# Kernel optimization log

Hardware: AMD Instinct MI355X
Metric: run time of the kernel (lower is better)

The kernel has to match this reference:

```python
import jax, jax.numpy as jnp
import numpy as np

QMAX = 127.0

def fake_quant(t):
    # per-tensor symmetric int8 quantize -> dequantize (STE for grads)
    scale = jnp.maximum(jnp.max(jnp.abs(t)) / QMAX, 1e-8)
    q = jnp.clip(jnp.round(t / scale), -QMAX, QMAX) * scale
    return t + jax.lax.stop_gradient(q - t)

def qlinear(x, W, b):
    # quantized linear: int8 activations x int8 weights, dequantized output
    return fake_quant(x) @ fake_quant(W).T + b

def hardsigmoid(t):
    return jnp.clip(t / 6.0 + 0.5, 0.0, 1.0)

def setup_inputs() -> dict:
    key = jax.random.key(0)
    ks = jax.random.split(key, 5)
    B, C, H, W_, R = 64, 1024, 28, 28, 256
    return {
        "x":  jax.random.normal(ks[0], (B, C, H, W_), dtype=jnp.float32),
        "W1": jax.random.normal(ks[1], (R, C), dtype=jnp.float32) * (1.0 / np.sqrt(C)),
        "b1": jax.random.normal(ks[2], (R,), dtype=jnp.float32) * 0.01,
        "W2": jax.random.normal(ks[3], (C, R), dtype=jnp.float32) * (1.0 / np.sqrt(R)),
        "b2": jax.random.normal(ks[4], (C,), dtype=jnp.float32) * 0.01,
    }

def reference(x, W1, b1, W2, b2):
    b, c, h, w = x.shape
    # 1. quantize input
    xq = fake_quant(x)
    # 2. quantized global avgpool -> [b, c]
    se = fake_quant(jnp.mean(xq, axis=(2, 3)))
    # 3-4. quantized fc1 -> fp32 relu
    se = jax.nn.relu(qlinear(se, W1, b1))
    # 5. quantized fc2 -> fp32
    se = qlinear(se, W2, b2)
    # 6. hardsigmoid gate
    se = hardsigmoid(se)
    # 7. broadcast scale in fp32 (original input path was fp32)
    return x * se[:, :, None, None]
```

## Files before the change

### kernel.cpp

```cpp
#include <hip/hip_runtime.h>

#define QMAX 127.0f
#define B_   64
#define C_   1024
#define HW_  784
#define R_   256
#define NROW 65536
#define N4_TOTAL 12845056
#define ROW4 196

typedef float fx4 __attribute__((ext_vector_type(4)));

#define PX_OFF   0
#define PW1_OFF  1024
#define PW2_OFF  2048
#define PM_OFF   3072
#define PH_OFF   4096
#define MEAN_OFF 8192
#define H_OFF    (MEAN_OFF + NROW)

__device__ __forceinline__ float block_max(float v, volatile float* sm) {
    #pragma unroll
    for (int o = 32; o > 0; o >>= 1) v = fmaxf(v, __shfl_xor(v, o, 64));
    int lane = threadIdx.x & 63, wid = threadIdx.x >> 6;
    if (lane == 0) sm[wid] = v;
    __syncthreads();
    float r = fmaxf(fmaxf(sm[0], sm[1]), fmaxf(sm[2], sm[3]));
    __syncthreads();
    return r;
}

__device__ __forceinline__ float amax4(float4 v) {
    return fmaxf(fmaxf(fabsf(v.x), fabsf(v.y)), fmaxf(fabsf(v.z), fabsf(v.w)));
}

__device__ __forceinline__ int q1(float v, float rs) {
    return (int)fminf(fmaxf(rintf(v * rs), -QMAX), QMAX);
}

__device__ __forceinline__ int q4sum(float4 v, float rs) {
    return q1(v.x, rs) + q1(v.y, rs) + q1(v.z, rs) + q1(v.w, rs);
}

__global__ __launch_bounds__(256) void kA(const float4* __restrict__ x,
                                          const float4* __restrict__ w1,
                                          const float4* __restrict__ w2,
                                          float* __restrict__ ws) {
    __shared__ float sm[4];
    int tid = blockIdx.x * 256 + threadIdx.x;
    float mx = 0.0f;
    #pragma unroll 7
    for (int j = 0; j < 49; j++) mx = fmaxf(mx, amax4(x[tid + j * 262144]));
    float m1 = (tid < 65536) ? amax4(w1[tid]) : 0.0f;
    float m2 = (tid < 65536) ? amax4(w2[tid]) : 0.0f;
    float bx  = block_max(mx, sm);
    float b1m = block_max(m1, sm);
    float b2m = block_max(m2, sm);
    if (threadIdx.x == 0) {
        ws[PX_OFF  + blockIdx.x] = bx;
        ws[PW1_OFF + blockIdx.x] = b1m;
        ws[PW2_OFF + blockIdx.x] = b2m;
    }
}

__global__ __launch_bounds__(256) void kB(const float* __restrict__ x,
                                          float* __restrict__ ws) {
    __shared__ float sm[4];
    int t = threadIdx.x;
    const float* px = ws + PX_OFF;
    float v = fmaxf(fmaxf(px[t], px[t + 256]), fmaxf(px[t + 512], px[t + 768]));
    float gmax = block_max(v, sm);
    float s  = fmaxf(gmax / QMAX, 1e-8f);
    float rs = 1.0f / s;
    int wid = t >> 6, lane = t & 63;
    int gw = blockIdx.x * 4 + wid;
    float wmax = 0.0f;
    #pragma unroll
    for (int k = 0; k < 8; k++) {
        int bc = gw * 8 + k;
        const float4* p = (const float4*)(x + (size_t)bc * HW_);
        int isum = 0;
        #pragma unroll
        for (int j = 0; j < 3; j++) isum += q4sum(p[lane + 64 * j], rs);
        if (lane < 4) isum += q4sum(p[192 + lane], rs);
        #pragma unroll
        for (int o = 32; o > 0; o >>= 1) isum += __shfl_xor(isum, o, 64);
        float m = (float)isum * s / 784.0f;
        if (lane == 0) ws[MEAN_OFF + bc] = m;
        wmax = fmaxf(wmax, fabsf(m));
    }
    float bm = block_max(wmax, sm);
    if (t == 0) ws[PM_OFF + blockIdx.x] = bm;
}

__global__ __launch_bounds__(256) void kC(const float* __restrict__ W1,
                                          const float* __restrict__ b1,
                                          float* __restrict__ ws) {
    __shared__ float sm[4];
    int t = threadIdx.x;
    const float* pm = ws + PM_OFF;
    const float* pw = ws + PW1_OFF;
    float vm = fmaxf(fmaxf(pm[t], pm[t + 256]), fmaxf(pm[t + 512], pm[t + 768]));
    float vw = fmaxf(fmaxf(pw[t], pw[t + 256]), fmaxf(pw[t + 512], pw[t + 768]));
    float mmax = block_max(vm, sm);
    float wmx  = block_max(vw, sm);
    float s2  = fmaxf(mmax / QMAX, 1e-8f);
    float s2q = fmaxf((QMAX * s2) / QMAX, 1e-8f);
    float sw  = fmaxf(wmx / QMAX, 1e-8f);
    float rs2 = 1.0f / s2, rsw = 1.0f / sw;
    int wid = t >> 6, lane = t & 63;
    int gw = blockIdx.x * 4 + wid;
    float hmax = 0.0f;
    #pragma unroll
    for (int k = 0; k < 4; k++) {
        int out = gw * 4 + k;
        int b = out >> 8, r = out & 255;
        const float4* mrow = (const float4*)(ws + MEAN_OFF + b * C_);
        const float4* wrow = (const float4*)(W1 + r * C_);
        int idot = 0;
        #pragma unroll
        for (int j = 0; j < 4; j++) {
            float4 mv = mrow[lane + 64 * j];
            float4 wv = wrow[lane + 64 * j];
            idot += q1(mv.x, rs2) * q1(wv.x, rsw) + q1(mv.y, rs2) * q1(wv.y, rsw)
                  + q1(mv.z, rs2) * q1(wv.z, rsw) + q1(mv.w, rs2) * q1(wv.w, rsw);
        }
        #pragma unroll
        for (int o = 32; o > 0; o >>= 1) idot += __shfl_xor(idot, o, 64);
        float hv = fmaxf((float)idot * (s2q * sw) + b1[r], 0.0f);
        if (lane == 0) ws[H_OFF + out] = hv;
        hmax = fmaxf(hmax, hv);
    }
    float bh = block_max(hmax, sm);
    if (t == 0) ws[PH_OFF + blockIdx.x] = bh;
}

__global__ __launch_bounds__(256) void kDE(const float* __restrict__ x,
                                           const float* __restrict__ W2,
                                           const float* __restrict__ b2,
                                           const float* __restrict__ ws,
                                           float* __restrict__ out) {
    __shared__ float sm[4];
    int t = threadIdx.x;
    const float* ph = ws + PH_OFF;
    const float* pw = ws + PW2_OFF;
    float vh = fmaxf(fmaxf(ph[t], ph[t + 256]), fmaxf(ph[t + 512], ph[t + 768]));
    float vw = fmaxf(fmaxf(pw[t], pw[t + 256]), fmaxf(pw[t + 512], pw[t + 768]));
    float hmx = block_max(vh, sm);
    float wmx = block_max(vw, sm);
    float sh = fmaxf(hmx / QMAX, 1e-8f);
    float sw = fmaxf(wmx / QMAX, 1e-8f);
    float rsh = 1.0f / sh, rsw = 1.0f / sw;
    int wid = t >> 6, lane = t & 63;
    int gw = blockIdx.x * 4 + wid;
    int bc0 = gw * 8;
    int b = bc0 >> 10;
    const float4* hrow = (const float4*)(ws + H_OFF + b * R_);
    float4 hv = hrow[lane];
    int qhx = q1(hv.x, rsh), qhy = q1(hv.y, rsh);
    int qhz = q1(hv.z, rsh), qhw = q1(hv.w, rsh);
    #pragma unroll
    for (int k = 0; k < 8; k++) {
        int bc = bc0 + k;
        int c = bc & 1023;
        const float4* wrow = (const float4*)(W2 + c * R_);
        float4 wv = wrow[lane];
        int idot = qhx * q1(wv.x, rsw) + qhy * q1(wv.y, rsw)
                 + qhz * q1(wv.z, rsw) + qhw * q1(wv.w, rsw);
        #pragma unroll
        for (int o = 32; o > 0; o >>= 1) idot += __shfl_xor(idot, o, 64);
        float tv = (float)idot * (sh * sw) + b2[c];
        float g = fminf(fmaxf(tv / 6.0f + 0.5f, 0.0f), 1.0f);
        const fx4* p = (const fx4*)(x + (size_t)bc * HW_);
        fx4* o4 = (fx4*)(out + (size_t)bc * HW_);
        #pragma unroll
        for (int j = 0; j < 3; j++) {
            fx4 v = p[lane + 64 * j];
            v *= g;
            __builtin_nontemporal_store(v, &o4[lane + 64 * j]);
        }
        if (lane < 4) {
            fx4 v = p[192 + lane];
            v *= g;
            __builtin_nontemporal_store(v, &o4[192 + lane]);
        }
    }
}

extern "C" void kernel_launch(void* const* d_in, const int* in_sizes, int n_in,
                              void* d_out, int out_size, void* d_ws, size_t ws_size,
                              hipStream_t stream) {
    const float* x  = (const float*)d_in[0];
    const float* W1 = (const float*)d_in[1];
    const float* b1 = (const float*)d_in[2];
    const float* W2 = (const float*)d_in[3];
    const float* b2 = (const float*)d_in[4];
    float* out = (float*)d_out;
    float* ws  = (float*)d_ws;

    kA <<<1024, 256, 0, stream>>>((const float4*)x, (const float4*)W1, (const float4*)W2, ws);
    kB <<<2048, 256, 0, stream>>>(x, ws);
    kC <<<1024, 256, 0, stream>>>(W1, b1, ws);
    kDE<<<2048, 256, 0, stream>>>(x, W2, b2, ws, out);
}
```

Measured before the change: 416.2 us.

## Fuse four stages into one persistent kernel with grid-wide atomic barriers

Replaces the four separate launches with a single persistent kernel of 512 blocks that runs absmax, quantized pooling, fc1 and fc2+gating in sequence, separated by spin-wait grid barriers on atomic counters reset by a memset. Each block now covers more rows per stage, and fc1 reuses quantized means held in registers across several outputs. Integer dot products become float FMAs. The aim is to remove kernel launch gaps and tail effects between stages. The risks are lower parallelism per stage, the cost of the barriers, and a deadlock if all 512 blocks are not co-resident on the device.

```diff
diff --git a/kernel.cpp b/kernel.cpp
--- a/kernel.cpp
+++ b/kernel.cpp
@@ -6,17 +6,17 @@
 #define HW_  784
 #define R_   256
 #define NROW 65536
-#define N4_TOTAL 12845056
-#define ROW4 196
+#define NBLK 512
 
 typedef float fx4 __attribute__((ext_vector_type(4)));
 
 #define PX_OFF   0
-#define PW1_OFF  1024
-#define PW2_OFF  2048
-#define PM_OFF   3072
-#define PH_OFF   4096
-#define MEAN_OFF 8192
+#define PW1_OFF  512
+#define PW2_OFF  1024
+#define PM_OFF   1536
+#define PH_OFF   2048
+#define CNT_OFF  2560
+#define MEAN_OFF 4096
 #define H_OFF    (MEAN_OFF + NROW)
 
 __device__ __forceinline__ float block_max(float v, volatile float* sm) {
@@ -34,155 +34,168 @@
     return fmaxf(fmaxf(fabsf(v.x), fabsf(v.y)), fmaxf(fabsf(v.z), fabsf(v.w)));
 }
 
-__device__ __forceinline__ int q1(float v, float rs) {
-    return (int)fminf(fmaxf(rintf(v * rs), -QMAX), QMAX);
-}
-
-__device__ __forceinline__ int q4sum(float4 v, float rs) {
-    return q1(v.x, rs) + q1(v.y, rs) + q1(v.z, rs) + q1(v.w, rs);
-}
-
-__global__ __launch_bounds__(256) void kA(const float4* __restrict__ x,
-                                          const float4* __restrict__ w1,
-                                          const float4* __restrict__ w2,
-                                          float* __restrict__ ws) {
+__device__ __forceinline__ float qf(float v, float rs) {
+    return fminf(fmaxf(rintf(v * rs), -QMAX), QMAX);
+}
+__device__ __forceinline__ float q4f(float4 v, float rs) {
+    return qf(v.x, rs) + qf(v.y, rs) + qf(v.z, rs) + qf(v.w, rs);
+}
+
+__device__ __forceinline__ void gsync(int* cnt, int target) {
+    __syncthreads();
+    if (threadIdx.x == 0) {
+        __threadfence();
+        __hip_atomic_fetch_add(cnt, 1, __ATOMIC_RELEASE, __HIP_MEMORY_SCOPE_AGENT);
+        while (__hip_atomic_load(cnt, __ATOMIC_ACQUIRE, __HIP_MEMORY_SCOPE_AGENT) < target)
+            __builtin_amdgcn_s_sleep(1);
+    }
+    __syncthreads();
+}
+
+__global__ __launch_bounds__(256, 2) void kFused(
+        const float* __restrict__ x,
+        const float* __restrict__ W1, const float* __restrict__ b1,
+        const float* __restrict__ W2, const float* __restrict__ b2,
+        float* __restrict__ ws, float* __restrict__ out)
+{
     __shared__ float sm[4];
-    int tid = blockIdx.x * 256 + threadIdx.x;
-    float mx = 0.0f;
-    #pragma unroll 7
-    for (int j = 0; j < 49; j++) mx = fmaxf(mx, amax4(x[tid + j * 262144]));
-    float m1 = (tid < 65536) ? amax4(w1[tid]) : 0.0f;
-    float m2 = (tid < 65536) ? amax4(w2[tid]) : 0.0f;
-    float bx  = block_max(mx, sm);
-    float b1m = block_max(m1, sm);
-    float b2m = block_max(m2, sm);
-    if (threadIdx.x == 0) {
-        ws[PX_OFF  + blockIdx.x] = bx;
-        ws[PW1_OFF + blockIdx.x] = b1m;
-        ws[PW2_OFF + blockIdx.x] = b2m;
-    }
-}
-
-__global__ __launch_bounds__(256) void kB(const float* __restrict__ x,
-                                          float* __restrict__ ws) {
-    __shared__ float sm[4];
-    int t = threadIdx.x;
-    const float* px = ws + PX_OFF;
-    float v = fmaxf(fmaxf(px[t], px[t + 256]), fmaxf(px[t + 512], px[t + 768]));
-    float gmax = block_max(v, sm);
-    float s  = fmaxf(gmax / QMAX, 1e-8f);
-    float rs = 1.0f / s;
-    int wid = t >> 6, lane = t & 63;
-    int gw = blockIdx.x * 4 + wid;
-    float wmax = 0.0f;
-    #pragma unroll
-    for (int k = 0; k < 8; k++) {
-        int bc = gw * 8 + k;
-        const float4* p = (const float4*)(x + (size_t)bc * HW_);
-        int isum = 0;
-        #pragma unroll
-        for (int j = 0; j < 3; j++) isum += q4sum(p[lane + 64 * j], rs);
-        if (lane < 4) isum += q4sum(p[192 + lane], rs);
-        #pragma unroll
-        for (int o = 32; o > 0; o >>= 1) isum += __shfl_xor(isum, o, 64);
-        float m = (float)isum * s / 784.0f;
-        if (lane == 0) ws[MEAN_OFF + bc] = m;
-        wmax = fmaxf(wmax, fabsf(m));
-    }
-    float bm = block_max(wmax, sm);
-    if (t == 0) ws[PM_OFF + blockIdx.x] = bm;
-}
-
-__global__ __launch_bounds__(256) void kC(const float* __restrict__ W1,
-                                          const float* __restrict__ b1,
-                                          float* __restrict__ ws) {
-    __shared__ float sm[4];
-    int t = threadIdx.x;
-    const float* pm = ws + PM_OFF;
-    const float* pw = ws + PW1_OFF;
-    float vm = fmaxf(fmaxf(pm[t], pm[t + 256]), fmaxf(pm[t + 512], pm[t + 768]));
-    float vw = fmaxf(fmaxf(pw[t], pw[t + 256]), fmaxf(pw[t + 512], pw[t + 768]));
-    float mmax = block_max(vm, sm);
-    float wmx  = block_max(vw, sm);
-    float s2  = fmaxf(mmax / QMAX, 1e-8f);
-    float s2q = fmaxf((QMAX * s2) / QMAX, 1e-8f);
-    float sw  = fmaxf(wmx / QMAX, 1e-8f);
-    float rs2 = 1.0f / s2, rsw = 1.0f / sw;
-    int wid = t >> 6, lane = t & 63;
-    int gw = blockIdx.x * 4 + wid;
-    float hmax = 0.0f;
-    #pragma unroll
-    for (int k = 0; k < 4; k++) {
-        int out = gw * 4 + k;
-        int b = out >> 8, r = out & 255;
+    const int t = threadIdx.x;
+    const int lane = t & 63, wid = t >> 6;
+    const int bid = blockIdx.x;
+    int* cnt = (int*)(ws + CNT_OFF);
+
+    {
+        const float4* x4 = (const float4*)x;
+        int tid = bid * 256 + t;
+        float mx = 0.0f;
+        #pragma unroll 7
+        for (int j = 0; j < 98; j++) mx = fmaxf(mx, amax4(x4[tid + j * 131072]));
+        float m1 = 0.0f, m2 = 0.0f;
+        if (tid < 65536) {
+            m1 = amax4(((const float4*)W1)[tid]);
+            m2 = amax4(((const float4*)W2)[tid]);
+        }
+        float bx = block_max(mx, sm);
+        float p1 = block_max(m1, sm);
+        float p2 = block_max(m2, sm);
+        if (t == 0) {
+            ws[PX_OFF  + bid] = bx;
+            ws[PW1_OFF + bid] = p1;
+            ws[PW2_OFF + bid] = p2;
+        }
+    }
+    gsync(cnt + 0, NBLK);
+
+    {
+        const float* px = ws + PX_OFF;
+        float gmax = block_max(fmaxf(px[t], px[t + 256]), sm);
+        float s  = fmaxf(gmax / QMAX, 1e-8f);
+        float rs = 1.0f / s;
+        int gw = bid * 4 + wid;
+        float wmax = 0.0f;
+        #pragma unroll 2
+        for (int k = 0; k < 32; k++) {
+            int bc = gw * 32 + k;
+            const float4* p = (const float4*)(x + (size_t)bc * HW_);
+            float fs = q4f(p[lane], rs) + q4f(p[lane + 64], rs) + q4f(p[lane + 128], rs);
+            if (lane < 4) fs += q4f(p[192 + lane], rs);
+            #pragma unroll
+            for (int o = 32; o > 0; o >>= 1) fs += __shfl_xor(fs, o, 64);
+            float m = fs * s / 784.0f;
+            if (lane == 0) ws[MEAN_OFF + bc] = m;
+            wmax = fmaxf(wmax, fabsf(m));
+        }
+        float bm = block_max(wmax, sm);
+        if (t == 0) ws[PM_OFF + bid] = bm;
+    }
+    gsync(cnt + 1, NBLK);
+
+    {
+        const float* pm = ws + PM_OFF;
+        const float* pw = ws + PW1_OFF;
+        float mmax = block_max(fmaxf(pm[t], pm[t + 256]), sm);
+        float wmx  = block_max(fmaxf(pw[t], pw[t + 256]), sm);
+        float s2 = fmaxf(mmax / QMAX, 1e-8f);
+        float sw = fmaxf(wmx / QMAX, 1e-8f);
+        float rs2 = 1.0f / s2, rsw = 1.0f / sw;
+        int gw = bid * 4 + wid;
+        int b = gw >> 5;
         const float4* mrow = (const float4*)(ws + MEAN_OFF + b * C_);
-        const float4* wrow = (const float4*)(W1 + r * C_);
-        int idot = 0;
+        float qm[16];
         #pragma unroll
         for (int j = 0; j < 4; j++) {
             float4 mv = mrow[lane + 64 * j];
-            float4 wv = wrow[lane + 64 * j];
-            idot += q1(mv.x, rs2) * q1(wv.x, rsw) + q1(mv.y, rs2) * q1(wv.y, rsw)
-                  + q1(mv.z, rs2) * q1(wv.z, rsw) + q1(mv.w, rs2) * q1(wv.w, rsw);
-        }
-        #pragma unroll
-        for (int o = 32; o > 0; o >>= 1) idot += __shfl_xor(idot, o, 64);
-        float hv = fmaxf((float)idot * (s2q * sw) + b1[r], 0.0f);
-        if (lane == 0) ws[H_OFF + out] = hv;
-        hmax = fmaxf(hmax, hv);
-    }
-    float bh = block_max(hmax, sm);
-    if (t == 0) ws[PH_OFF + blockIdx.x] = bh;
-}
-
-__global__ __launch_bounds__(256) void kDE(const float* __restrict__ x,
-                                           const float* __restrict__ W2,
-                                           const float* __restrict__ b2,
-                                           const float* __restrict__ ws,
-                                           float* __restrict__ out) {
-    __shared__ float sm[4];
-    int t = threadIdx.x;
-    const float* ph = ws + PH_OFF;
-    const float* pw = ws + PW2_OFF;
-    float vh = fmaxf(fmaxf(ph[t], ph[t + 256]), fmaxf(ph[t + 512], ph[t + 768]));
-    float vw = fmaxf(fmaxf(pw[t], pw[t + 256]), fmaxf(pw[t + 512], pw[t + 768]));
-    float hmx = block_max(vh, sm);
-    float wmx = block_max(vw, sm);
-    float sh = fmaxf(hmx / QMAX, 1e-8f);
-    float sw = fmaxf(wmx / QMAX, 1e-8f);
-    float rsh = 1.0f / sh, rsw = 1.0f / sw;
-    int wid = t >> 6, lane = t & 63;
-    int gw = blockIdx.x * 4 + wid;
-    int bc0 = gw * 8;
-    int b = bc0 >> 10;
-    const float4* hrow = (const float4*)(ws + H_OFF + b * R_);
-    float4 hv = hrow[lane];
-    int qhx = q1(hv.x, rsh), qhy = q1(hv.y, rsh);
-    int qhz = q1(hv.z, rsh), qhw = q1(hv.w, rsh);
-    #pragma unroll
-    for (int k = 0; k < 8; k++) {
-        int bc = bc0 + k;
-        int c = bc & 1023;
-        const float4* wrow = (const float4*)(W2 + c * R_);
-        float4 wv = wrow[lane];
-        int idot = qhx * q1(wv.x, rsw) + qhy * q1(wv.y, rsw)
-                 + qhz * q1(wv.z, rsw) + qhw * q1(wv.w, rsw);
-        #pragma unroll
-        for (int o = 32; o > 0; o >>= 1) idot += __shfl_xor(idot, o, 64);
-        float tv = (float)idot * (sh * sw) + b2[c];
-        float g = fminf(fmaxf(tv / 6.0f + 0.5f, 0.0f), 1.0f);
-        const fx4* p = (const fx4*)(x + (size_t)bc * HW_);
-        fx4* o4 = (fx4*)(out + (size_t)bc * HW_);
-        #pragma unroll
-        for (int j = 0; j < 3; j++) {
-            fx4 v = p[lane + 64 * j];
-            v *= g;
-            __builtin_nontemporal_store(v, &o4[lane + 64 * j]);
-        }
-        if (lane < 4) {
-            fx4 v = p[192 + lane];
-            v *= g;
-            __builtin_nontemporal_store(v, &o4[192 + lane]);
+            qm[4*j+0] = qf(mv.x, rs2); qm[4*j+1] = qf(mv.y, rs2);
+            qm[4*j+2] = qf(mv.z, rs2); qm[4*j+3] = qf(mv.w, rs2);
+        }
+        float hmax = 0.0f;
+        #pragma unroll 2
+        for (int k = 0; k < 8; k++) {
+            int outn = gw * 8 + k;
+            int r = outn & 255;
+            const float4* wrow = (const float4*)(W1 + r * C_);
+            float fdot = 0.0f;
+            #pragma unroll
+            for (int j = 0; j < 4; j++) {
+                float4 wv = wrow[lane + 64 * j];
+                fdot = fmaf(qm[4*j+0], qf(wv.x, rsw), fdot);
+                fdot = fmaf(qm[4*j+1], qf(wv.y, rsw), fdot);
+                fdot = fmaf(qm[4*j+2], qf(wv.z, rsw), fdot);
+                fdot = fmaf(qm[4*j+3], qf(wv.w, rsw), fdot);
+            }
+            #pragma unroll
+            for (int o = 32; o > 0; o >>= 1) fdot += __shfl_xor(fdot, o, 64);
+            float hv = fmaxf(fdot * (s2 * sw) + b1[r], 0.0f);
+            if (lane == 0) ws[H_OFF + outn] = hv;
+            hmax = fmaxf(hmax, hv);
+        }
+        float bh = block_max(hmax, sm);
+        if (t == 0) ws[PH_OFF + bid] = bh;
+    }
+    gsync(cnt + 2, NBLK);
+
+    {
+        const float* ph = ws + PH_OFF;
+        const float* pw = ws + PW2_OFF;
+        float hmx = block_max(fmaxf(ph[t], ph[t + 256]), sm);
+        float wmx = block_max(fmaxf(pw[t], pw[t + 256]), sm);
+        float sh = fmaxf(hmx / QMAX, 1e-8f);
+        float sw = fmaxf(wmx / QMAX, 1e-8f);
+        float rsh = 1.0f / sh, rsw = 1.0f / sw;
+        int gw = bid * 4 + wid;
+        int bc0 = gw * 32;
+        int b = gw >> 5;
+        const float4* hrow = (const float4*)(ws + H_OFF + b * R_);
+        float4 hv4 = hrow[lane];
+        float qh_x = qf(hv4.x, rsh), qh_y = qf(hv4.y, rsh);
+        float qh_z = qf(hv4.z, rsh), qh_w = qf(hv4.w, rsh);
+        #pragma unroll 2
+        for (int k = 0; k < 32; k++) {
+            int bc = bc0 + k;
+            int c = bc & 1023;
+            const float4* wrow = (const float4*)(W2 + c * R_);
+            float4 wv = wrow[lane];
+            float fdot =      qh_x * qf(wv.x, rsw);
+            fdot = fmaf(qh_y, qf(wv.y, rsw), fdot);
+            fdot = fmaf(qh_z, qf(wv.z, rsw), fdot);
+            fdot = fmaf(qh_w, qf(wv.w, rsw), fdot);
+            #pragma unroll
+            for (int o = 32; o > 0; o >>= 1) fdot += __shfl_xor(fdot, o, 64);
+            float tv = fdot * (sh * sw) + b2[c];
+            float g = fminf(fmaxf(tv / 6.0f + 0.5f, 0.0f), 1.0f);
+            const fx4* p = (const fx4*)(x + (size_t)bc * HW_);
+            fx4* o4 = (fx4*)(out + (size_t)bc * HW_);
+            #pragma unroll
+            for (int j = 0; j < 3; j++) {
+                fx4 v = p[lane + 64 * j];
+                v *= g;
+                __builtin_nontemporal_store(v, &o4[lane + 64 * j]);
+            }
+            if (lane < 4) {
+                fx4 v = p[192 + lane];
+                v *= g;
+                __builtin_nontemporal_store(v, &o4[192 + lane]);
+            }
         }
     }
 }
@@ -198,8 +211,6 @@
     float* out = (float*)d_out;
     float* ws  = (float*)d_ws;
 
-    kA <<<1024, 256, 0, stream>>>((const float4*)x, (const float4*)W1, (const float4*)W2, ws);
-    kB <<<2048, 256, 0, stream>>>(x, ws);
-    kC <<<1024, 256, 0, stream>>>(W1, b1, ws);
-    kDE<<<2048, 256, 0, stream>>>(x, W2, b2, ws, out);
-}
+    hipMemsetAsync((char*)d_ws + CNT_OFF * 4, 0, 16, stream);
+    kFused<<<NBLK, 256, 0, stream>>>(x, W1, b1, W2, b2, ws, out);
+}
```

Result: slower. 564.2 us (+35.5%).
